# Performance work log

Measured on AMD Instinct MI355X. Metric: run time of the kernel, lower is better.

Reference implementation:

```python
import jax, jax.numpy as jnp
import numpy as np

B, S, D_MODEL, H, D_KV = 2, 2048, 1024, 16, 64
NUM_BUCKETS, MAX_DIST = 32, 128


def _relative_position_bucket(rel_pos, num_buckets=NUM_BUCKETS, max_distance=MAX_DIST):
    # bidirectional (encoder) bucketing, matching T5Attention._relative_position_bucket
    nb = num_buckets // 2
    buckets = (rel_pos > 0).astype(jnp.int32) * nb
    rel = jnp.abs(rel_pos)
    max_exact = nb // 2
    is_small = rel < max_exact
    rel_f = jnp.maximum(rel.astype(jnp.float32), 1.0)  # guard log(0); masked by is_small anyway
    large = max_exact + (
        jnp.log(rel_f / max_exact) / np.log(max_distance / max_exact) * (nb - max_exact)
    ).astype(jnp.int32)
    large = jnp.minimum(large, nb - 1)
    return buckets + jnp.where(is_small, rel, large)


def setup_inputs() -> dict:
    key = jax.random.key(0)
    ks = jax.random.split(key, 6)
    sc = 1.0 / np.sqrt(D_MODEL)
    return {
        "hidden_states": jax.random.normal(ks[0], (B, S, D_MODEL), jnp.float32),
        "Wq": jax.random.normal(ks[1], (D_MODEL, H * D_KV), jnp.float32) * sc,
        "Wk": jax.random.normal(ks[2], (D_MODEL, H * D_KV), jnp.float32) * sc,
        "Wv": jax.random.normal(ks[3], (D_MODEL, H * D_KV), jnp.float32) * sc,
        "Wo": jax.random.normal(ks[4], (H * D_KV, D_MODEL), jnp.float32) * sc,
        "rel_bias_table": jax.random.normal(ks[5], (NUM_BUCKETS, H), jnp.float32),
    }


def reference(hidden_states, Wq, Wk, Wv, Wo, rel_bias_table):
    b, s, _ = hidden_states.shape
    # projections (T5 uses no bias, scale=1.0 in attention)
    q = (hidden_states @ Wq).reshape(b, s, H, D_KV).transpose(0, 2, 1, 3)  # bhsd
    k = (hidden_states @ Wk).reshape(b, s, H, D_KV).transpose(0, 2, 1, 3)
    v = (hidden_states @ Wv).reshape(b, s, H, D_KV).transpose(0, 2, 1, 3)

    # relative position bias: [1, H, S, S]
    ctx = jnp.arange(s)[:, None]
    mem = jnp.arange(s)[None, :]
    buckets = _relative_position_bucket(mem - ctx)          # [S, S]
    pos_bias = rel_bias_table[buckets]                       # [S, S, H]
    pos_bias = pos_bias.transpose(2, 0, 1)[None]             # [1, H, S, S]

    scores = jnp.einsum("bhqd,bhkd->bhqk", q, k) + pos_bias  # scale = 1.0
    probs = jax.nn.softmax(scores, axis=-1)
    attn = jnp.einsum("bhqk,bhkd->bhqd", probs, v)
    attn = attn.transpose(0, 2, 1, 3).reshape(b, s, H * D_KV)
    return attn @ Wo
```

## Files before the change

kernel.cpp:

```cpp
#include <hip/hip_runtime.h>
#include <hip/hip_fp16.h>

#define S_LEN 2048
#define NH 16
#define DK 64
#define DM 1024
#define NB 2
#define QKV_SZ (NB * NH * S_LEN * DK)
#define HSTRIDE (S_LEN * DK)

typedef _Float16 half8 __attribute__((ext_vector_type(8)));
typedef _Float16 half4v __attribute__((ext_vector_type(4)));
typedef __fp16 fp16x2 __attribute__((ext_vector_type(2)));
typedef float f32x4 __attribute__((ext_vector_type(4)));

static __device__ __forceinline__ half4v pack4(const f32x4 v) {
  fp16x2 lo = __builtin_amdgcn_cvt_pkrtz(v[0], v[1]);
  fp16x2 hi = __builtin_amdgcn_cvt_pkrtz(v[2], v[3]);
  half4v r;
  ((fp16x2*)&r)[0] = lo;
  ((fp16x2*)&r)[1] = hi;
  return r;
}

#define GLL(gp, lp)                                                              \
  __builtin_amdgcn_global_load_lds(                                              \
      (const __attribute__((address_space(1))) unsigned int*)(gp),               \
      (__attribute__((address_space(3))) unsigned int*)(lp), 16, 0, 0)


__global__ __launch_bounds__(256) void prep_kernel(
    const float* __restrict__ hs, const float* __restrict__ Wq,
    const float* __restrict__ Wk, const float* __restrict__ Wv,
    const float* __restrict__ Wo, _Float16* __restrict__ Xh,
    _Float16* __restrict__ Wqkvt, _Float16* __restrict__ Wot,
    const float* __restrict__ table, float* __restrict__ btab) {
  int z = blockIdx.z;
  int tx = threadIdx.x, ty = threadIdx.y;
  if (z >= 5) {
    int i = (((z - 5) << 10) + (int)(blockIdx.y * 32 + blockIdx.x)) * 256 + ty * 32 + tx;
    float4 v = ((const float4*)hs)[i];
    half4v o;
    o[0] = (_Float16)v.x; o[1] = (_Float16)v.y; o[2] = (_Float16)v.z; o[3] = (_Float16)v.w;
    ((half4v*)Xh)[i] = o;
    return;
  }
  if (z == 4) {
    int i = (int)(blockIdx.y * 32 + blockIdx.x) * 256 + ty * 32 + tx;
    if (i >= NH * 4095) return;
    int h = i / 4095, r = i - h * 4095;
    int rel = r - 2047;
    int bucket = rel > 0 ? 16 : 0;
    int a = rel < 0 ? -rel : rel;
    if (a < 8) {
      bucket += a;
    } else {
      int lg = 31 - __clz(a * a);
      int large = 8 + (lg - 6);
      bucket += (large < 15 ? large : 15);
    }
    btab[i] = table[bucket * NH + h] * 1.44269504f;
    return;
  }
  __shared__ float tile[32][33];
  const float* W = (z == 0) ? Wq : (z == 1) ? Wk : (z == 2) ? Wv : Wo;
  _Float16* Wt = (z < 3) ? (Wqkvt + (size_t)z * 1048576) : Wot;
  float scale = (z == 0) ? 1.44269504f : 1.0f;
  int nx = blockIdx.x * 32 + tx;
  int ky = blockIdx.y * 32;
#pragma unroll
  for (int i = 0; i < 32; i += 8) tile[ty + i][tx] = W[(size_t)(ky + ty + i) * DM + nx];
  __syncthreads();
  int kx = ky + tx;
  int ny = blockIdx.x * 32;
#pragma unroll
  for (int i = 0; i < 32; i += 8)
    Wt[(size_t)(ny + ty + i) * DM + kx] = (_Float16)(tile[tx][ty + i] * scale);
}

__global__ __launch_bounds__(256) void gemm_qkv(const _Float16* __restrict__ A,
                                                const _Float16* __restrict__ Bt,
                                                _Float16* __restrict__ QKV) {
  __shared__ _Float16 As[128 * 32];
  __shared__ _Float16 Bs[128 * 32];
  const int K = DM;
  const int t = threadIdx.x;
  const int m0 = blockIdx.y * 128, n0 = blockIdx.x * 128;
  const int w = t >> 6, lane = t & 63, l15 = lane & 15, quad = lane >> 4;
  const int wr = (w >> 1) * 64, wc = (w & 1) * 64;
  const int swz = (quad ^ (l15 & 3)) * 8;
  const bool swapped = (n0 < 2048);

  f32x4 acc[4][4];
#pragma unroll
  for (int i = 0; i < 4; i++)
#pragma unroll
    for (int j = 0; j < 4; j++) acc[i][j] = (f32x4){0.f, 0.f, 0.f, 0.f};

  for (int k0 = 0; k0 < K; k0 += 32) {
    __syncthreads();
#pragma unroll
    for (int i = 0; i < 2; i++) {
      int id = t + 256 * i;
      int row = id >> 2, c = id & 3;
      int cg = c ^ (row & 3);
      GLL(A + (size_t)(m0 + row) * K + k0 + cg * 8, (char*)As + id * 16);
      GLL(Bt + (size_t)(n0 + row) * K + k0 + cg * 8, (char*)Bs + id * 16);
    }
    __syncthreads();
    half8 af[4], bf[4];
#pragma unroll
    for (int i = 0; i < 4; i++) af[i] = *(const half8*)(As + (wr + i * 16 + l15) * 32 + swz);
#pragma unroll
    for (int i = 0; i < 4; i++) bf[i] = *(const half8*)(Bs + (wc + i * 16 + l15) * 32 + swz);
    if (swapped) {
#pragma unroll
      for (int i = 0; i < 4; i++)
#pragma unroll
        for (int j = 0; j < 4; j++)
          acc[i][j] = __builtin_amdgcn_mfma_f32_16x16x32_f16(bf[j], af[i], acc[i][j], 0, 0, 0);
    } else {
#pragma unroll
      for (int i = 0; i < 4; i++)
#pragma unroll
        for (int j = 0; j < 4; j++)
          acc[i][j] = __builtin_amdgcn_mfma_f32_16x16x32_f16(af[i], bf[j], acc[i][j], 0, 0, 0);
    }
  }

#pragma unroll
  for (int i = 0; i < 4; i++)
#pragma unroll
    for (int j = 0; j < 4; j++) {
      if (swapped) {
        int srow = m0 + wr + i * 16 + l15;
        int col0 = n0 + wc + j * 16 + quad * 4;
        int which = col0 >> 10, rem = col0 & 1023, hh = rem >> 6, dd = rem & 63;
        int bb = srow >> 11, ss = srow & 2047;
        int lin = ((ss >> 4) << 10) + (((dd >> 5) * 4 + ((dd >> 3) & 3)) << 7) +
                  ((ss & 15) << 3) + (dd & 7);
        *(half4v*)(QKV + (size_t)which * QKV_SZ + (size_t)(bb * NH + hh) * HSTRIDE + lin) =
            pack4(acc[i][j]);
      } else {
        int row0 = m0 + wr + i * 16 + quad * 4;
        int col = n0 + wc + j * 16 + l15;
        int rem = col & 1023, hh = rem >> 6, dd = rem & 63;
        int bb = row0 >> 11, ss = row0 & 2047;
        int lin = ((ss >> 6) << 12) +
                  ((((dd >> 4) * 2 + ((ss >> 5) & 1)) * 4 + ((ss >> 3) & 3)) << 7) +
                  ((dd & 15) << 3) + (ss & 7);
        *(half4v*)(QKV + (size_t)2 * QKV_SZ + (size_t)(bb * NH + hh) * HSTRIDE + lin) =
            pack4(acc[i][j]);
      }
    }
}

__global__ __launch_bounds__(256, 4) void attn_kernel(
    const _Float16* __restrict__ Qf, const _Float16* __restrict__ Kf,
    const _Float16* __restrict__ Vf, const float* __restrict__ btab,
    _Float16* __restrict__ attn_out) {
  __shared__ _Float16 Ps[4][1024];
  __shared__ float slab[512];

  const int t = threadIdx.x;
  const int Q0 = blockIdx.x * 64;
  const int h = blockIdx.y, b = blockIdx.z;
  const int w = t >> 6, lane = t & 63, l15 = lane & 15, quad = lane >> 4;
  const int qw0 = Q0 + w * 16;
  const int sw7 = l15 & 7;
  const size_t hb = (size_t)(b * NH + h) * HSTRIDE;
  const _Float16* Qb = Qf + hb;
  const _Float16* Kb = Kf + hb;
  const _Float16* Vb = Vf + hb;

  for (int i = t; i < 512; i += 256) slab[i] = btab[h * 4095 + 1791 + i];

  half8 qf[2];
  {
    const _Float16* Qt = Qb + (qw0 >> 4) * 1024 + l15 * 8;
    qf[0] = *(const half8*)(Qt + quad * 128);
    qf[1] = *(const half8*)(Qt + (4 + quad) * 128);
  }

  f32x4 o[4];
#pragma unroll
  for (int dt = 0; dt < 4; dt++) o[dt] = (f32x4){0.f, 0.f, 0.f, 0.f};
  float m_ = -INFINITY, l_ = 0.f;

  __syncthreads();

  for (int k0 = 0; k0 < S_LEN; k0 += 64) {
    half8 kf[4][2], vf[4][2];
    const _Float16* Kc = Kb + (k0 >> 4) * 1024 + l15 * 8;
    const _Float16* Vc = Vb + (k0 >> 6) * 4096 + l15 * 8;
#pragma unroll
    for (int kt = 0; kt < 4; kt++) {
      kf[kt][0] = *(const half8*)(Kc + kt * 1024 + quad * 128);
      kf[kt][1] = *(const half8*)(Kc + kt * 1024 + (4 + quad) * 128);
    }
#pragma unroll
    for (int dt = 0; dt < 4; dt++) {
      vf[dt][0] = *(const half8*)(Vc + (dt * 8 + quad) * 128);
      vf[dt][1] = *(const half8*)(Vc + (dt * 8 + 4 + quad) * 128);
    }

    const int dk0 = k0 - qw0;
    const bool farneg = (dk0 <= -191);
    const bool farpos = (dk0 >= 143);
    const bool nearc = !(farneg || farpos);
    const float cb = farneg ? slab[128] : slab[384];

    f32x4 st[4];
    if (nearc) {
#pragma unroll
      for (int kt = 0; kt < 4; kt++) {
        int i0 = dk0 + kt * 16 + quad * 4 - l15 + 256;
        f32x4 v;
        v[0] = slab[i0]; v[1] = slab[i0 + 1]; v[2] = slab[i0 + 2]; v[3] = slab[i0 + 3];
        st[kt] = v;
      }
    } else {
#pragma unroll
      for (int kt = 0; kt < 4; kt++) st[kt] = (f32x4){0.f, 0.f, 0.f, 0.f};
    }

#pragma unroll
    for (int kt = 0; kt < 4; kt++)
#pragma unroll
      for (int dh = 0; dh < 2; dh++)
        st[kt] = __builtin_amdgcn_mfma_f32_16x16x32_f16(kf[kt][dh], qf[dh], st[kt], 0, 0, 0);

    float cm = fmaxf(fmaxf(st[0][0], st[0][1]), fmaxf(st[0][2], st[0][3]));
#pragma unroll
    for (int kt = 1; kt < 4; kt++)
      cm = fmaxf(cm, fmaxf(fmaxf(st[kt][0], st[kt][1]), fmaxf(st[kt][2], st[kt][3])));
    cm = fmaxf(cm, __shfl_xor(cm, 16));
    cm = fmaxf(cm, __shfl_xor(cm, 32));
    float mc = nearc ? cm : cm + cb;
    if (__any(mc > m_)) {
      float mnew = fmaxf(m_, mc);
      float alpha = __builtin_amdgcn_exp2f(m_ - mnew);
      m_ = mnew;
      l_ *= alpha;
#pragma unroll
      for (int dt = 0; dt < 4; dt++) o[dt] *= alpha;
    }
    float msub = nearc ? m_ : m_ - cb;

    f32x4 lacc = (f32x4){0.f, 0.f, 0.f, 0.f};
#pragma unroll
    for (int kt = 0; kt < 4; kt++) {
      f32x4 p;
#pragma unroll
      for (int r = 0; r < 4; r++) p[r] = __builtin_amdgcn_exp2f(st[kt][r] - msub);
      lacc += p;
      int g = 2 * kt + (quad >> 1);
      *(half4v*)(&Ps[w][l15 * 64 + ((g ^ sw7) << 3) + ((quad & 1) << 2)]) = pack4(p);
    }
    l_ += (lacc[0] + lacc[1]) + (lacc[2] + lacc[3]);
    __asm__ volatile("s_waitcnt lgkmcnt(0)" ::: "memory");

    half8 pf[2];
#pragma unroll
    for (int kh = 0; kh < 2; kh++)
      pf[kh] = *(const half8*)(&Ps[w][l15 * 64 + ((((kh << 2) + quad) ^ sw7) << 3)]);
#pragma unroll
    for (int dt = 0; dt < 4; dt++)
#pragma unroll
      for (int kh = 0; kh < 2; kh++)
        o[dt] = __builtin_amdgcn_mfma_f32_16x16x32_f16(vf[dt][kh], pf[kh], o[dt], 0, 0, 0);
  }

  float lf = l_;
  lf += __shfl_xor(lf, 16);
  lf += __shfl_xor(lf, 32);
  float inv = 1.0f / lf;
  int q = qw0 + l15;
#pragma unroll
  for (int dt = 0; dt < 4; dt++) {
    f32x4 ov = o[dt] * inv;
    *(half4v*)(attn_out + ((size_t)(b * S_LEN + q)) * DM + h * DK + dt * 16 + quad * 4) =
        pack4(ov);
  }
}

__global__ __launch_bounds__(256) void gemm_out(const _Float16* __restrict__ A,
                                                const _Float16* __restrict__ Bt,
                                                float* __restrict__ C) {
  __shared__ _Float16 As[64 * 32];
  __shared__ _Float16 Bs[64 * 32];
  const int K = DM, N = DM;
  const int t = threadIdx.x;
  const int m0 = blockIdx.y * 64, n0 = blockIdx.x * 64;
  const int w = t >> 6, lane = t & 63, l15 = lane & 15, quad = lane >> 4;
  const int wr = (w >> 1) * 32, wc = (w & 1) * 32;
  const int swz = (quad ^ (l15 & 3)) * 8;

  f32x4 acc[2][2];
#pragma unroll
  for (int i = 0; i < 2; i++)
#pragma unroll
    for (int j = 0; j < 2; j++) acc[i][j] = (f32x4){0.f, 0.f, 0.f, 0.f};

  for (int k0 = 0; k0 < K; k0 += 32) {
    __syncthreads();
    {
      int row = t >> 2, c = t & 3;
      int cg = c ^ (row & 3);
      GLL(A + (size_t)(m0 + row) * K + k0 + cg * 8, (char*)As + t * 16);
      GLL(Bt + (size_t)(n0 + row) * K + k0 + cg * 8, (char*)Bs + t * 16);
    }
    __syncthreads();
    half8 af[2], bf[2];
#pragma unroll
    for (int i = 0; i < 2; i++) af[i] = *(const half8*)(As + (wr + i * 16 + l15) * 32 + swz);
#pragma unroll
    for (int j = 0; j < 2; j++) bf[j] = *(const half8*)(Bs + (wc + j * 16 + l15) * 32 + swz);
#pragma unroll
    for (int i = 0; i < 2; i++)
#pragma unroll
      for (int j = 0; j < 2; j++)
        acc[i][j] = __builtin_amdgcn_mfma_f32_16x16x32_f16(bf[j], af[i], acc[i][j], 0, 0, 0);
  }

#pragma unroll
  for (int i = 0; i < 2; i++)
#pragma unroll
    for (int j = 0; j < 2; j++) {
      int srow = m0 + wr + i * 16 + l15;
      int col0 = n0 + wc + j * 16 + quad * 4;
      *(f32x4*)(C + (size_t)srow * N + col0) = acc[i][j];
    }
}

extern "C" void kernel_launch(void* const* d_in, const int* in_sizes, int n_in,
                              void* d_out, int out_size, void* d_ws, size_t ws_size,
                              hipStream_t stream) {
  const float* hs  = (const float*)d_in[0];
  const float* Wq  = (const float*)d_in[1];
  const float* Wk  = (const float*)d_in[2];
  const float* Wv  = (const float*)d_in[3];
  const float* Wo  = (const float*)d_in[4];
  const float* tbl = (const float*)d_in[5];
  float* out = (float*)d_out;
  char* ws = (char*)d_ws;

  _Float16* Xh    = (_Float16*)(ws);
  _Float16* Wqkvt = (_Float16*)(ws + (8u << 20));
  _Float16* Wot   = (_Float16*)(ws + (14u << 20));
  _Float16* Qd    = (_Float16*)(ws + (16u << 20));
  _Float16* Ah    = (_Float16*)(ws + (40u << 20));
  float*    btab  = (float*)(ws + (48u << 20));
  _Float16* Kd    = Qd + (size_t)QKV_SZ;
  _Float16* Vd    = Qd + (size_t)2 * QKV_SZ;

  prep_kernel<<<dim3(32, 32, 9), dim3(32, 8), 0, stream>>>(hs, Wq, Wk, Wv, Wo, Xh,
                                                           Wqkvt, Wot, tbl, btab);
  gemm_qkv<<<dim3(24, 32), 256, 0, stream>>>(Xh, Wqkvt, Qd);
  attn_kernel<<<dim3(S_LEN / 64, NH, NB), 256, 0, stream>>>(Qd, Kd, Vd, btab, Ah);
  gemm_out<<<dim3(16, 64), 256, 0, stream>>>(Ah, Wot, out);
}
```

Before: 219.8 us.

## Double-buffer V tiles in LDS and prefetch next K tile into registers

The attention kernel now stages each 64-key V tile into a double-buffered shared-memory array with asynchronous global-to-LDS loads, shared by all four waves in the block. It also software-pipelines K by loading the next tile's fragments into a second register set while the current tile is processed. The goal is to hide global load latency behind the MFMA and softmax work and to stop each wave from fetching V on its own. In exchange it adds a block-wide barrier every iteration, extra LDS use, and more registers, and it lowers the occupancy hint from 4 to 3 blocks per CU.

```diff
diff --git a/kernel.cpp b/kernel.cpp
--- a/kernel.cpp
+++ b/kernel.cpp
@@ -155,10 +155,11 @@
     }
 }
 
-__global__ __launch_bounds__(256, 4) void attn_kernel(
+__global__ __launch_bounds__(256, 3) void attn_kernel(
     const _Float16* __restrict__ Qf, const _Float16* __restrict__ Kf,
     const _Float16* __restrict__ Vf, const float* __restrict__ btab,
     _Float16* __restrict__ attn_out) {
+  __shared__ _Float16 Vs[2][4096];
   __shared__ _Float16 Ps[4][1024];
   __shared__ float slab[512];
 
@@ -182,6 +183,20 @@
     qf[1] = *(const half8*)(Qt + (4 + quad) * 128);
   }
 
+  GLL(Vb + t * 8, &Vs[0][t * 8]);
+  GLL(Vb + 2048 + t * 8, &Vs[0][t * 8 + 2048]);
+
+  const _Float16* kp = Kb + quad * 128 + l15 * 8;
+
+  half8 kfa[4][2], kfb[4][2];
+#define LOADK(dst, base)                                                   \
+  {                                                                        \
+    _Pragma("unroll") for (int kt_ = 0; kt_ < 4; kt_++)                    \
+      _Pragma("unroll") for (int dh_ = 0; dh_ < 2; dh_++)                  \
+        dst[kt_][dh_] = *(const half8*)((base) + kt_ * 1024 + dh_ * 512);  \
+  }
+  LOADK(kfa, kp);
+
   f32x4 o[4];
 #pragma unroll
   for (int dt = 0; dt < 4; dt++) o[dt] = (f32x4){0.f, 0.f, 0.f, 0.f};
@@ -189,22 +204,15 @@
 
   __syncthreads();
 
-  for (int k0 = 0; k0 < S_LEN; k0 += 64) {
-    half8 kf[4][2], vf[4][2];
-    const _Float16* Kc = Kb + (k0 >> 4) * 1024 + l15 * 8;
-    const _Float16* Vc = Vb + (k0 >> 6) * 4096 + l15 * 8;
-#pragma unroll
-    for (int kt = 0; kt < 4; kt++) {
-      kf[kt][0] = *(const half8*)(Kc + kt * 1024 + quad * 128);
-      kf[kt][1] = *(const half8*)(Kc + kt * 1024 + (4 + quad) * 128);
-    }
-#pragma unroll
-    for (int dt = 0; dt < 4; dt++) {
-      vf[dt][0] = *(const half8*)(Vc + (dt * 8 + quad) * 128);
-      vf[dt][1] = *(const half8*)(Vc + (dt * 8 + 4 + quad) * 128);
-    }
-
-    const int dk0 = k0 - qw0;
+  auto process = [&](int it, int bi, half8 kcur[4][2], half8 knxt[4][2]) {
+    if (it + 1 < 32) {
+      const _Float16* vsrc = Vb + (it + 1) * 4096 + t * 8;
+      GLL(vsrc, &Vs[bi ^ 1][t * 8]);
+      GLL(vsrc + 2048, &Vs[bi ^ 1][t * 8 + 2048]);
+      LOADK(knxt, kp + (it + 1) * 4096);
+    }
+
+    const int dk0 = it * 64 - qw0;
     const bool farneg = (dk0 <= -191);
     const bool farpos = (dk0 >= 143);
     const bool nearc = !(farneg || farpos);
@@ -228,7 +236,7 @@
     for (int kt = 0; kt < 4; kt++)
 #pragma unroll
       for (int dh = 0; dh < 2; dh++)
-        st[kt] = __builtin_amdgcn_mfma_f32_16x16x32_f16(kf[kt][dh], qf[dh], st[kt], 0, 0, 0);
+        st[kt] = __builtin_amdgcn_mfma_f32_16x16x32_f16(kcur[kt][dh], qf[dh], st[kt], 0, 0, 0);
 
     float cm = fmaxf(fmaxf(st[0][0], st[0][1]), fmaxf(st[0][2], st[0][3]));
 #pragma unroll
@@ -260,7 +268,7 @@
     l_ += (lacc[0] + lacc[1]) + (lacc[2] + lacc[3]);
     __asm__ volatile("s_waitcnt lgkmcnt(0)" ::: "memory");
 
-    half8 pf[2];
+    half8 pf[2], vf[4][2];
 #pragma unroll
     for (int kh = 0; kh < 2; kh++)
       pf[kh] = *(const half8*)(&Ps[w][l15 * 64 + ((((kh << 2) + quad) ^ sw7) << 3)]);
@@ -268,8 +276,21 @@
     for (int dt = 0; dt < 4; dt++)
 #pragma unroll
       for (int kh = 0; kh < 2; kh++)
+        vf[dt][kh] = *(const half8*)(&Vs[bi][(dt * 8 + kh * 4 + quad) * 128 + l15 * 8]);
+#pragma unroll
+    for (int dt = 0; dt < 4; dt++)
+#pragma unroll
+      for (int kh = 0; kh < 2; kh++)
         o[dt] = __builtin_amdgcn_mfma_f32_16x16x32_f16(vf[dt][kh], pf[kh], o[dt], 0, 0, 0);
-  }
+
+    __syncthreads();
+  };
+
+  for (int it = 0; it < 32; it += 2) {
+    process(it, 0, kfa, kfb);
+    process(it + 1, 1, kfb, kfa);
+  }
+#undef LOADK
 
   float lf = l_;
   lf += __shfl_xor(lf, 16);
```

New measurement: 219.5 us. No clear change (-0.1%).

## Split attention over keys across warps with in-block softmax merge

Applied to the files above, without the earlier changes.

Each warp now handles all 64 queries of the block but only a quarter of the key range (split-K flash attention). K and V fragments loaded from global memory are reused across four query tiles instead of being loaded separately by every warp. Partial max, sum and output accumulators are merged through shared memory at the end. This cuts redundant K/V global traffic per block. The cost is more registers (occupancy hint lowered to 3 blocks), more shared memory, and a multi-sync reduction epilogue.

```diff
diff --git a/kernel.cpp b/kernel.cpp
--- a/kernel.cpp
+++ b/kernel.cpp
@@ -155,18 +155,20 @@
     }
 }
 
-__global__ __launch_bounds__(256, 4) void attn_kernel(
+__global__ __launch_bounds__(256, 3) void attn_kernel(
     const _Float16* __restrict__ Qf, const _Float16* __restrict__ Kf,
     const _Float16* __restrict__ Vf, const float* __restrict__ btab,
     _Float16* __restrict__ attn_out) {
-  __shared__ _Float16 Ps[4][1024];
-  __shared__ float slab[512];
+  __shared__ __align__(16) char smem[36864];
+  _Float16* Ps = (_Float16*)smem;
+  float* slab = (float*)(smem + 32768);
+  float* obuf = (float*)smem;
+  float* mlbuf = (float*)(smem + 34816);
 
   const int t = threadIdx.x;
   const int Q0 = blockIdx.x * 64;
   const int h = blockIdx.y, b = blockIdx.z;
   const int w = t >> 6, lane = t & 63, l15 = lane & 15, quad = lane >> 4;
-  const int qw0 = Q0 + w * 16;
   const int sw7 = l15 & 7;
   const size_t hb = (size_t)(b * NH + h) * HSTRIDE;
   const _Float16* Qb = Qf + hb;
@@ -175,113 +177,190 @@
 
   for (int i = t; i < 512; i += 256) slab[i] = btab[h * 4095 + 1791 + i];
 
-  half8 qf[2];
-  {
-    const _Float16* Qt = Qb + (qw0 >> 4) * 1024 + l15 * 8;
-    qf[0] = *(const half8*)(Qt + quad * 128);
-    qf[1] = *(const half8*)(Qt + (4 + quad) * 128);
-  }
-
-  f32x4 o[4];
-#pragma unroll
-  for (int dt = 0; dt < 4; dt++) o[dt] = (f32x4){0.f, 0.f, 0.f, 0.f};
-  float m_ = -INFINITY, l_ = 0.f;
-
-  __syncthreads();
-
-  for (int k0 = 0; k0 < S_LEN; k0 += 64) {
-    half8 kf[4][2], vf[4][2];
-    const _Float16* Kc = Kb + (k0 >> 4) * 1024 + l15 * 8;
-    const _Float16* Vc = Vb + (k0 >> 6) * 4096 + l15 * 8;
-#pragma unroll
-    for (int kt = 0; kt < 4; kt++) {
-      kf[kt][0] = *(const half8*)(Kc + kt * 1024 + quad * 128);
-      kf[kt][1] = *(const half8*)(Kc + kt * 1024 + (4 + quad) * 128);
-    }
-#pragma unroll
-    for (int dt = 0; dt < 4; dt++) {
-      vf[dt][0] = *(const half8*)(Vc + (dt * 8 + quad) * 128);
-      vf[dt][1] = *(const half8*)(Vc + (dt * 8 + 4 + quad) * 128);
-    }
-
-    const int dk0 = k0 - qw0;
-    const bool farneg = (dk0 <= -191);
-    const bool farpos = (dk0 >= 143);
-    const bool nearc = !(farneg || farpos);
-    const float cb = farneg ? slab[128] : slab[384];
-
-    f32x4 st[4];
-    if (nearc) {
+  half8 qf[4][2];
+#pragma unroll
+  for (int qt = 0; qt < 4; qt++)
+#pragma unroll
+    for (int dh = 0; dh < 2; dh++)
+      qf[qt][dh] = *(const half8*)(Qb + ((Q0 >> 4) + qt) * 1024 + (dh * 4 + quad) * 128 +
+                                   l15 * 8);
+
+  f32x4 o[4][4];
+#pragma unroll
+  for (int dt = 0; dt < 4; dt++)
+#pragma unroll
+    for (int qt = 0; qt < 4; qt++) o[dt][qt] = (f32x4){0.f, 0.f, 0.f, 0.f};
+  float m_[4] = {-INFINITY, -INFINITY, -INFINITY, -INFINITY};
+  float l_[4] = {0.f, 0.f, 0.f, 0.f};
+
+  _Float16* Pw = Ps + w * 4096;
+
+  __syncthreads();
+
+  for (int it = 0; it < 8; it++) {
+    const int ks0 = (w << 9) + (it << 6);
+    const _Float16* Kc = Kb + ks0 * 64;
+    const _Float16* Vc = Vb + ks0 * 64;
+
+    half8 kf[4][2];
+#pragma unroll
+    for (int kt = 0; kt < 4; kt++)
+#pragma unroll
+      for (int dh = 0; dh < 2; dh++)
+        kf[kt][dh] = *(const half8*)(Kc + kt * 1024 + (dh * 4 + quad) * 128 + l15 * 8);
+
+#pragma unroll
+    for (int qt = 0; qt < 4; qt++) {
+      const int dkq = ks0 - Q0 - qt * 16;
+      const bool farneg = (dkq <= -191);
+      const bool farpos = (dkq >= 143);
+      const bool nearc = !(farneg || farpos);
+      const float cb = farneg ? slab[128] : slab[384];
+
+      f32x4 st[4];
+      if (nearc) {
+#pragma unroll
+        for (int kt = 0; kt < 4; kt++) {
+          int i0 = dkq + kt * 16 + quad * 4 - l15 + 256;
+          f32x4 v;
+          v[0] = slab[i0]; v[1] = slab[i0 + 1]; v[2] = slab[i0 + 2]; v[3] = slab[i0 + 3];
+          st[kt] = v;
+        }
+      } else {
+#pragma unroll
+        for (int kt = 0; kt < 4; kt++) st[kt] = (f32x4){0.f, 0.f, 0.f, 0.f};
+      }
+#pragma unroll
+      for (int kt = 0; kt < 4; kt++)
+#pragma unroll
+        for (int dh = 0; dh < 2; dh++)
+          st[kt] = __builtin_amdgcn_mfma_f32_16x16x32_f16(kf[kt][dh], qf[qt][dh], st[kt],
+                                                          0, 0, 0);
+
+      float cm = fmaxf(fmaxf(st[0][0], st[0][1]), fmaxf(st[0][2], st[0][3]));
+#pragma unroll
+      for (int kt = 1; kt < 4; kt++)
+        cm = fmaxf(cm, fmaxf(fmaxf(st[kt][0], st[kt][1]), fmaxf(st[kt][2], st[kt][3])));
+      cm = fmaxf(cm, __shfl_xor(cm, 16));
+      cm = fmaxf(cm, __shfl_xor(cm, 32));
+      float mc = nearc ? cm : cm + cb;
+      if (__any(mc > m_[qt])) {
+        float mnew = fmaxf(m_[qt], mc);
+        float alpha = __builtin_amdgcn_exp2f(m_[qt] - mnew);
+        m_[qt] = mnew;
+        l_[qt] *= alpha;
+#pragma unroll
+        for (int dt = 0; dt < 4; dt++) o[dt][qt] *= alpha;
+      }
+      float msub = nearc ? m_[qt] : m_[qt] - cb;
+
+      f32x4 lacc = (f32x4){0.f, 0.f, 0.f, 0.f};
 #pragma unroll
       for (int kt = 0; kt < 4; kt++) {
-        int i0 = dk0 + kt * 16 + quad * 4 - l15 + 256;
-        f32x4 v;
-        v[0] = slab[i0]; v[1] = slab[i0 + 1]; v[2] = slab[i0 + 2]; v[3] = slab[i0 + 3];
-        st[kt] = v;
+        f32x4 p;
+#pragma unroll
+        for (int r = 0; r < 4; r++) p[r] = __builtin_amdgcn_exp2f(st[kt][r] - msub);
+        lacc += p;
+        int g = 2 * kt + (quad >> 1);
+        *(half4v*)(&Pw[qt * 1024 + l15 * 64 + ((g ^ sw7) << 3) + ((quad & 1) << 2)]) =
+            pack4(p);
       }
-    } else {
-#pragma unroll
-      for (int kt = 0; kt < 4; kt++) st[kt] = (f32x4){0.f, 0.f, 0.f, 0.f};
-    }
-
-#pragma unroll
-    for (int kt = 0; kt < 4; kt++)
-#pragma unroll
-      for (int dh = 0; dh < 2; dh++)
-        st[kt] = __builtin_amdgcn_mfma_f32_16x16x32_f16(kf[kt][dh], qf[dh], st[kt], 0, 0, 0);
-
-    float cm = fmaxf(fmaxf(st[0][0], st[0][1]), fmaxf(st[0][2], st[0][3]));
-#pragma unroll
-    for (int kt = 1; kt < 4; kt++)
-      cm = fmaxf(cm, fmaxf(fmaxf(st[kt][0], st[kt][1]), fmaxf(st[kt][2], st[kt][3])));
-    cm = fmaxf(cm, __shfl_xor(cm, 16));
-    cm = fmaxf(cm, __shfl_xor(cm, 32));
-    float mc = nearc ? cm : cm + cb;
-    if (__any(mc > m_)) {
-      float mnew = fmaxf(m_, mc);
-      float alpha = __builtin_amdgcn_exp2f(m_ - mnew);
-      m_ = mnew;
-      l_ *= alpha;
-#pragma unroll
-      for (int dt = 0; dt < 4; dt++) o[dt] *= alpha;
-    }
-    float msub = nearc ? m_ : m_ - cb;
-
-    f32x4 lacc = (f32x4){0.f, 0.f, 0.f, 0.f};
-#pragma unroll
-    for (int kt = 0; kt < 4; kt++) {
-      f32x4 p;
-#pragma unroll
-      for (int r = 0; r < 4; r++) p[r] = __builtin_amdgcn_exp2f(st[kt][r] - msub);
-      lacc += p;
-      int g = 2 * kt + (quad >> 1);
-      *(half4v*)(&Ps[w][l15 * 64 + ((g ^ sw7) << 3) + ((quad & 1) << 2)]) = pack4(p);
-    }
-    l_ += (lacc[0] + lacc[1]) + (lacc[2] + lacc[3]);
+      l_[qt] += (lacc[0] + lacc[1]) + (lacc[2] + lacc[3]);
+    }
     __asm__ volatile("s_waitcnt lgkmcnt(0)" ::: "memory");
 
-    half8 pf[2];
-#pragma unroll
-    for (int kh = 0; kh < 2; kh++)
-      pf[kh] = *(const half8*)(&Ps[w][l15 * 64 + ((((kh << 2) + quad) ^ sw7) << 3)]);
+    half8 vf[4][2];
 #pragma unroll
     for (int dt = 0; dt < 4; dt++)
 #pragma unroll
       for (int kh = 0; kh < 2; kh++)
-        o[dt] = __builtin_amdgcn_mfma_f32_16x16x32_f16(vf[dt][kh], pf[kh], o[dt], 0, 0, 0);
-  }
-
-  float lf = l_;
-  lf += __shfl_xor(lf, 16);
-  lf += __shfl_xor(lf, 32);
-  float inv = 1.0f / lf;
-  int q = qw0 + l15;
-#pragma unroll
-  for (int dt = 0; dt < 4; dt++) {
-    f32x4 ov = o[dt] * inv;
-    *(half4v*)(attn_out + ((size_t)(b * S_LEN + q)) * DM + h * DK + dt * 16 + quad * 4) =
-        pack4(ov);
-  }
+        vf[dt][kh] = *(const half8*)(Vc + ((dt * 2 + kh) * 4 + quad) * 128 + l15 * 8);
+#pragma unroll
+    for (int qt = 0; qt < 4; qt++) {
+      half8 pf[2];
+#pragma unroll
+      for (int kh = 0; kh < 2; kh++)
+        pf[kh] = *(const half8*)(&Pw[qt * 1024 + l15 * 64 +
+                                     ((((kh << 2) + quad) ^ sw7) << 3)]);
+#pragma unroll
+      for (int dt = 0; dt < 4; dt++)
+#pragma unroll
+        for (int kh = 0; kh < 2; kh++)
+          o[dt][qt] = __builtin_amdgcn_mfma_f32_16x16x32_f16(vf[dt][kh], pf[kh], o[dt][qt],
+                                                             0, 0, 0);
+    }
+  }
+
+#pragma unroll
+  for (int qt = 0; qt < 4; qt++) {
+    l_[qt] += __shfl_xor(l_[qt], 16);
+    l_[qt] += __shfl_xor(l_[qt], 32);
+  }
+  __syncthreads();
+  if (quad == 0) {
+#pragma unroll
+    for (int qt = 0; qt < 4; qt++) {
+      mlbuf[(w * 2 + 0) * 64 + qt * 16 + l15] = m_[qt];
+      mlbuf[(w * 2 + 1) * 64 + qt * 16 + l15] = l_[qt];
+    }
+  }
+  __syncthreads();
+  float aw[4], invL[4];
+#pragma unroll
+  for (int qt = 0; qt < 4; qt++) {
+    int q = qt * 16 + l15;
+    float M = mlbuf[0 * 64 + q];
+#pragma unroll
+    for (int v = 1; v < 4; v++) M = fmaxf(M, mlbuf[(v * 2) * 64 + q]);
+    float L = 0.f;
+#pragma unroll
+    for (int v = 0; v < 4; v++)
+      L += mlbuf[(v * 2 + 1) * 64 + q] * __builtin_amdgcn_exp2f(mlbuf[(v * 2) * 64 + q] - M);
+    aw[qt] = __builtin_amdgcn_exp2f(m_[qt] - M);
+    invL[qt] = 1.0f / L;
+  }
+#pragma unroll
+  for (int dt = 0; dt < 4; dt++)
+#pragma unroll
+    for (int qt = 0; qt < 4; qt++) o[dt][qt] *= aw[qt];
+
+#define OIDX(dt, qt) (((qt) * 16 + l15) * 68 + (dt) * 16 + quad * 4)
+  if (w & 1) {
+    float* ob = obuf + (w >> 1) * 4352;
+#pragma unroll
+    for (int dt = 0; dt < 4; dt++)
+#pragma unroll
+      for (int qt = 0; qt < 4; qt++) *(f32x4*)(&ob[OIDX(dt, qt)]) = o[dt][qt];
+  }
+  __syncthreads();
+  if (!(w & 1)) {
+    float* ob = obuf + (w >> 1) * 4352;
+#pragma unroll
+    for (int dt = 0; dt < 4; dt++)
+#pragma unroll
+      for (int qt = 0; qt < 4; qt++) o[dt][qt] += *(f32x4*)(&ob[OIDX(dt, qt)]);
+  }
+  __syncthreads();
+  if (w == 2) {
+#pragma unroll
+    for (int dt = 0; dt < 4; dt++)
+#pragma unroll
+      for (int qt = 0; qt < 4; qt++) *(f32x4*)(&obuf[OIDX(dt, qt)]) = o[dt][qt];
+  }
+  __syncthreads();
+  if (w == 0) {
+#pragma unroll
+    for (int qt = 0; qt < 4; qt++) {
+      int q = Q0 + qt * 16 + l15;
+#pragma unroll
+      for (int dt = 0; dt < 4; dt++) {
+        f32x4 ov = (o[dt][qt] + *(f32x4*)(&obuf[OIDX(dt, qt)])) * invL[qt];
+        *(half4v*)(attn_out + ((size_t)(b * S_LEN + q)) * DM + h * DK + dt * 16 + quad * 4) =
+            pack4(ov);
+      }
+    }
+  }
+#undef OIDX
 }
 
 __global__ __launch_bounds__(256) void gemm_out(const _Float16* __restrict__ A,
```

Measured after the change: 310.9 us. +41.5%, slower.
